# Kernel tuning notes

Measured on AMD Instinct MI355X. Metric: run time of the kernel, lower is better.

## Reference

```python
import jax, jax.numpy as jnp
import numpy as np

STRIDE = 16
SIZES = np.array([128.0, 256.0, 512.0], np.float32)
RATIOS = np.array([0.5, 1.0, 2.0], np.float32)
N_POS, N_NEG = 32, 32          # n_sample=64, pos_ratio=0.5
POS_THR, NEG_THR = 0.7, 0.2
W_CONF, W_REG = 1.0, 5.0


def _conv(x, w, b, stride, pad):
    y = jax.lax.conv_general_dilated(x, w, (stride, stride), [(pad, pad), (pad, pad)],
                                     dimension_numbers=('NCHW', 'OIHW', 'NCHW'))
    return y + b[None, :, None, None]


def _anchors(fw, fh, stride):
    # 9 anchors per center: 3 sizes x 3 aspect ratios
    ws = (SIZES[:, None] * np.sqrt(RATIOS)[None, :]).reshape(-1)
    hs = (SIZES[:, None] / np.sqrt(RATIOS)[None, :]).reshape(-1)
    wh = jnp.asarray(np.stack([ws, hs], -1))                      # (9,2)
    cx = (jnp.arange(fw, dtype=jnp.float32) + 0.5) * stride
    cy = (jnp.arange(fh, dtype=jnp.float32) + 0.5) * stride
    gx, gy = jnp.meshgrid(cx, cy, indexing='ij')                  # x-major, like the torch list comp
    ctr = jnp.stack([gx, gy], -1)[:, :, None, :]                  # (fw,fh,1,2)
    tl = ctr - wh / 2.0
    xywh = jnp.concatenate([tl, jnp.broadcast_to(wh, tl.shape)], -1)  # (fw,fh,9,4)
    return xywh.reshape(-1, 4)


def _xywh_to_xyxy(b):
    return jnp.concatenate([b[:, :2], b[:, :2] + b[:, 2:]], -1)


def _iou(a, b):  # a [N,4], b [M,4], xyxy
    lt = jnp.maximum(a[:, None, :2], b[None, :, :2])
    rb = jnp.minimum(a[:, None, 2:], b[None, :, 2:])
    inter = jnp.clip(rb - lt, 0.0).prod(-1)
    aa = (a[:, 2] - a[:, 0]) * (a[:, 3] - a[:, 1])
    ab = (b[:, 2] - b[:, 0]) * (b[:, 3] - b[:, 1])
    return inter / (aa[:, None] + ab[None, :] - inter)


def _head_flat(y, per):  # [1, 9*per, H, W] -> [W*H*9, per], matching anchor flatten order
    _, _, H, W = y.shape
    return y[0].reshape(9, per, H, W).transpose(3, 2, 0, 1).reshape(-1, per)


def _apply_offsets(boxes, off):  # decode proposals from xyxy boxes + (dx,dy,dw,dh)
    w = boxes[:, 2] - boxes[:, 0]; h = boxes[:, 3] - boxes[:, 1]
    cx = boxes[:, 0] + 0.5 * w;    cy = boxes[:, 1] + 0.5 * h
    ncx = cx + off[:, 0] * w;      ncy = cy + off[:, 1] * h
    nw = w * jnp.exp(off[:, 2]);   nh = h * jnp.exp(off[:, 3])
    return jnp.stack([ncx - nw / 2, ncy - nh / 2, ncx + nw / 2, ncy + nh / 2], -1)


def _box_offset(anc, gt):
    aw = anc[:, 2] - anc[:, 0]; ah = anc[:, 3] - anc[:, 1]
    acx = anc[:, 0] + 0.5 * aw; acy = anc[:, 1] + 0.5 * ah
    gw = gt[:, 2] - gt[:, 0];   gh = gt[:, 3] - gt[:, 1]
    gcx = gt[:, 0] + 0.5 * gw;  gcy = gt[:, 1] + 0.5 * gh
    return jnp.stack([(gcx - acx) / aw, (gcy - acy) / ah,
                      jnp.log(gw / aw), jnp.log(gh / ah)], -1)


def setup_inputs():
    key = jax.random.key(0)
    ks = jax.random.split(key, 12)
    img_data = jax.random.normal(ks[0], (1, 3, 1600, 1600), jnp.float32)
    x1 = jax.random.uniform(ks[1], (64,), minval=0.0, maxval=1400.0)
    y1 = jax.random.uniform(ks[2], (64,), minval=0.0, maxval=1400.0)
    bw = jax.random.uniform(ks[3], (64,), minval=32.0, maxval=200.0)
    bh = jax.random.uniform(ks[4], (64,), minval=32.0, maxval=200.0)
    gt_boxes = jnp.stack([x1, y1, x1 + bw, y1 + bh], -1)[None]   # [1,64,4], all valid (no -1 pad)
    gt_classes = jax.random.randint(ks[5], (1, 64), 1, 21, jnp.int32)
    def w(k, shape, fan):
        return jax.random.normal(k, shape, jnp.float32) * np.float32(np.sqrt(2.0 / fan))
    return dict(
        img_data=img_data, gt_boxes=gt_boxes, gt_classes=gt_classes,
        w1=w(ks[6], (64, 3, 7, 7), 3 * 49),      b1=jnp.zeros(64, jnp.float32),
        w2=w(ks[7], (256, 64, 3, 3), 64 * 9),    b2=jnp.zeros(256, jnp.float32),
        w_rpn=w(ks[8], (256, 256, 3, 3), 256 * 9), b_rpn=jnp.zeros(256, jnp.float32),
        w_cls=w(ks[9], (18, 256, 1, 1), 256),    b_cls=jnp.zeros(18, jnp.float32),
        w_reg=w(ks[10], (36, 256, 1, 1), 256),   b_reg=jnp.zeros(36, jnp.float32),
    )


def reference(img_data, gt_boxes, gt_classes, w1, b1, w2, b2, w_rpn, b_rpn, w_cls, b_cls, w_reg, b_reg):
    # --- feature extractor (total stride 16) ---
    fm = jax.nn.relu(_conv(img_data, w1, b1, 4, 3))
    fm = jax.nn.relu(_conv(fm, w2, b2, 4, 1))            # [1,256,100,100]
    H, W = fm.shape[2], fm.shape[3]
    # --- anchors + IoU matching ---
    anchors_xywh = _anchors(W, H, STRIDE)                # [N,4] xywh
    anchors_xyxy = _xywh_to_xyxy(anchors_xywh)
    gt = gt_boxes[0]                                     # [M,4], all valid
    ious = _iou(anchors_xyxy, gt)                        # [N,M]
    N = ious.shape[0]
    gt_max = ious.max(0)                                 # best iou per gt
    is_gt_best = (ious == gt_max[None, :]).any(1)        # torch: where(iou == gt_max)[0]
    anc_argmax = ious.argmax(1)
    anc_max = ious.max(1)
    labels = jnp.full((N,), -1.0, jnp.float32)
    labels = jnp.where(anc_max < NEG_THR, 0.0, labels)
    labels = jnp.where(is_gt_best, 1.0, labels)
    labels = jnp.where(anc_max > POS_THR, 1.0, labels)
    # --- deterministic pos/neg sampling (fixed sizes; replaces randperm subsampling) ---
    idx = jnp.arange(N, dtype=jnp.float32)
    _, pos_index = jax.lax.top_k(jnp.where(labels == 1.0, anc_max, -1.0), N_POS)
    _, neg_index = jax.lax.top_k(jnp.where(labels == 0.0, 1e6 - idx, -1e9), N_NEG)
    bboxes_pos = anchors_xyxy[pos_index]                 # box_convert(xywh->xyxy) of pos anchors
    # --- proposal module (RPN head) ---
    h = jax.nn.relu(_conv(fm, w_rpn, b_rpn, 1, 1))
    cls = _head_flat(_conv(h, w_cls, b_cls, 1, 0), 2)    # [N,2]
    reg = _head_flat(_conv(h, w_reg, b_reg, 1, 0), 4)    # [N,4]
    pos_score = cls[pos_index]
    neg_score = cls[neg_index]
    offset_pos = reg[pos_index]
    proposals = _apply_offsets(bboxes_pos, offset_pos)
    # --- losses ---
    gt_offset = _box_offset(bboxes_pos, gt[anc_argmax[pos_index]])
    logits = jnp.concatenate([pos_score, neg_score], 0)  # [64,2]
    tgt = jnp.concatenate([jnp.ones(N_POS, jnp.int32), jnp.zeros(N_NEG, jnp.int32)])
    logp = jax.nn.log_softmax(logits, -1)
    cls_loss = -logp[jnp.arange(N_POS + N_NEG), tgt].mean()
    d = gt_offset - offset_pos
    ad = jnp.abs(d)
    reg_loss = jnp.where(ad < 1.0, 0.5 * d * d, ad - 0.5).mean()
    total_rpn_loss = W_CONF * cls_loss + W_REG * reg_loss
    gt_cls_pos = gt_classes[0][anc_argmax[pos_index]]
    return (total_rpn_loss, fm, proposals, pos_index, gt_cls_pos)
```

## Files before the change

kernel.cpp:

```cpp
#include <hip/hip_runtime.h>
#include <math.h>


#define CAP 4096

typedef __attribute__((ext_vector_type(8))) short bf16x8;
typedef __attribute__((ext_vector_type(4))) float f32x4;

__device__ __forceinline__ void dma16(const void* g, void* l) {
    __builtin_amdgcn_global_load_lds((const __attribute__((address_space(1))) void*)g,
                                     (__attribute__((address_space(3))) void*)l, 16, 0, 0);
}

#define OFF_F1T     0
#define OFF_FMT     5171328
#define OFF_CPART   6503040
#define OFF_RPART   7223040
#define OFF_WA1     8663040
#define OFF_W9_2    8672448
#define OFF_W9_3    8746176
#define OFF_WTC     9041088
#define OFF_WTG     9045696
#define OFF_AARG    9054912
#define OFF_NEGM    9144912
#define OFF_POSM    9147728
#define OFF_GTMAX   9150544
#define OFF_CANDS   9150688
#define OFF_CANDI   9154784
#define OFF_IMGB    9158880

__device__ __forceinline__ unsigned short f2bf(float f) {
    unsigned int u = __float_as_uint(f);
    u += 0x7fffu + ((u >> 16) & 1u);
    return (unsigned short)(u >> 16);
}

__device__ __forceinline__ void anchor_box(int i, float& x0, float& y0,
                                           float& x1, float& y1, float& area) {
#pragma clang fp contract(off)
    const float sizes[3]  = {128.f, 256.f, 512.f};
    const float ratios[3] = {0.5f, 1.f, 2.f};
    int a = i % 9;
    int q = i / 9;
    int iy = q % 100;
    int ix = q / 100;
    int s = a / 3, r = a % 3;
    float sq = sqrtf(ratios[r]);
    float w = sizes[s] * sq;
    float h = sizes[s] / sq;
    float cx = ((float)ix + 0.5f) * 16.0f;
    float cy = ((float)iy + 0.5f) * 16.0f;
    x0 = cx - w * 0.5f;
    y0 = cy - h * 0.5f;
    x1 = x0 + w;
    y1 = y0 + h;
    area = (x1 - x0) * (y1 - y0);
}

__device__ __forceinline__ float iou_one(float ax0, float ay0, float ax1, float ay1, float aa,
                                         float bx0, float by0, float bx1, float by1, float ab) {
#pragma clang fp contract(off)
    float ltx = fmaxf(ax0, bx0), lty = fmaxf(ay0, by0);
    float rbx = fminf(ax1, bx1), rby = fminf(ay1, by1);
    float iw = fmaxf(rbx - ltx, 0.0f);
    float ih = fmaxf(rby - lty, 0.0f);
    float inter = iw * ih;
    return inter / ((aa + ab) - inter);
}

__global__ __launch_bounds__(256) void setup_kernel(const float* __restrict__ wc, float* __restrict__ wtc,
                                                    const float* __restrict__ wg, float* __restrict__ wtg,
                                                    const float* __restrict__ w1, unsigned short* __restrict__ wa1,
                                                    const float* __restrict__ w2, unsigned short* __restrict__ w9_2,
                                                    const float* __restrict__ wr, unsigned short* __restrict__ w9_3,
                                                    unsigned int* __restrict__ f1t_u, unsigned int* __restrict__ fmt_u,
                                                    unsigned int* __restrict__ gtmax,
                                                    const float* __restrict__ img, unsigned short* __restrict__ imgb) {
    int i = blockIdx.x * 256 + threadIdx.x;
    if (i < 65) { gtmax[i] = 0u; return; }
    i -= 65;
    if (i < 103040) {
        if (i < 51328) {
            int p = i >> 5, part = i & 31;
            int x, y;
            if (p < 804) { y = (p < 402) ? 0 : 401; x = p % 402; }
            else { int j = p - 804; x = (j < 400) ? 0 : 401; y = 1 + (j % 400); }
            f1t_u[(y * 402 + x) * 32 + part] = 0u;
        } else {
            int i2 = i - 51328;
            int p = i2 >> 7, part = i2 & 127;
            int x, y;
            if (p < 204) { y = (p < 102) ? 0 : 101; x = p % 102; }
            else { int j = p - 204; x = (j < 100) ? 0 : 101; y = 1 + (j % 100); }
            fmt_u[(y * 102 + x) * 128 + part] = 0u;
        }
        return;
    }
    i -= 103040;
    if (i < 4608) { int c = i / 256, k = i - c * 256; wtc[k * 18 + c] = wc[i]; return; }
    i -= 4608;
    if (i < 9216) { int c = i / 256, k = i - c * 256; wtg[k * 36 + c] = wg[i]; return; }
    i -= 9216;
    if (i < 12288) {
        int oc = i / 192, k = i - oc * 192;
        int q = k >> 3, kx = k & 7;
        int ky = q / 3, ic = q - (q / 3) * 3;
        wa1[i] = (q < 21 && kx < 7) ? f2bf(w1[oc * 147 + ic * 49 + ky * 7 + kx])
                                    : (unsigned short)0;
        return;
    }
    i -= 12288;
    if (i < 147456) {
        int unit = i >> 13;
        int rem = i & 8191;
        int ocT = rem >> 9;
        int rem2 = rem & 511;
        int lane = rem2 >> 3;
        int e = rem2 & 7;
        int cc = unit >> 1, kcl = unit & 1;
        int oc = ocT * 16 + (lane & 15);
        int ic = kcl * 32 + (lane >> 4) * 8 + e;
        w9_2[i] = f2bf(w2[(oc * 64 + ic) * 9 + cc]);
        return;
    }
    i -= 147456;
    if (i < 589824) {
        int unit = i >> 13;
        int rem = i & 8191;
        int ocT = rem >> 9;
        int rem2 = rem & 511;
        int lane = rem2 >> 3;
        int e = rem2 & 7;
        int cc = unit >> 1, kcl = unit & 1;
        int kk = cc >> 2, chv = cc & 3;
        int oc = ocT * 16 + (lane & 15);
        int icl = kcl * 32 + (lane >> 4) * 8 + e;
        w9_3[i] = f2bf(wr[(oc * 256 + chv * 64 + icl) * 9 + kk]);
        return;
    }
    i -= 589824;
    if (i < 974448) {
        int ic = i / 324816;
        int rem = i - ic * 324816;
        int row = rem / 202;
        int k = rem - row * 202;
        int y = row - 3;
        bool yok = (y >= 0) && (y < 1600);
        int yc = min(max(y, 0), 1599);
        const float* srow = img + ((size_t)(ic * 1600 + yc)) * 1600;
        unsigned int d[4];
#pragma unroll
        for (int e2 = 0; e2 < 4; e2++) {
            int x0 = k * 8 + 2 * e2 - 11;
            int x1 = x0 + 1;
            bool ok0 = yok && (x0 >= 0) && (x0 < 1600);
            bool ok1 = yok && (x1 >= 0) && (x1 < 1600);
            float f0 = srow[min(max(x0, 0), 1599)];
            float f1 = srow[min(max(x1, 0), 1599)];
            unsigned int lo = ok0 ? (unsigned int)f2bf(f0) : 0u;
            unsigned int hi = ok1 ? (unsigned int)f2bf(f1) : 0u;
            d[e2] = lo | (hi << 16);
        }
        *(uint4*)(imgb + ((size_t)(ic * 1608 + row)) * 1616 + k * 8) =
            make_uint4(d[0], d[1], d[2], d[3]);
    }
}

__device__ __forceinline__ void iou1_body(int bid, int t, const float* __restrict__ gt,
                                          int* __restrict__ aarg, unsigned int* __restrict__ gtmax) {
    __shared__ float sg1[64][4];
    __shared__ float sarea1[64];
    __shared__ unsigned int smax1[64];
    if (t < 64) {
#pragma clang fp contract(off)
        float b0 = gt[t * 4 + 0], b1 = gt[t * 4 + 1];
        float b2 = gt[t * 4 + 2], b3 = gt[t * 4 + 3];
        sg1[t][0] = b0; sg1[t][1] = b1; sg1[t][2] = b2; sg1[t][3] = b3;
        sarea1[t] = (b2 - b0) * (b3 - b1);
        smax1[t] = 0u;
    }
    __syncthreads();
    int i = bid * 256 + t;
    int iq = min(i, 89999);
    float x0, y0, x1, y1, aa;
    anchor_box(iq, x0, y0, x1, y1, aa);
    float best = -1.f;
    int bestj = 0;
    for (int j = 0; j < 64; j++) {
        float v = iou_one(x0, y0, x1, y1, aa, sg1[j][0], sg1[j][1], sg1[j][2], sg1[j][3], sarea1[j]);
        if (v > best) { best = v; bestj = j; }
        if (v > __uint_as_float(smax1[j])) atomicMax(&smax1[j], __float_as_uint(v));
    }
    if (i < 90000) aarg[i] = bestj;
    __syncthreads();
    if (t < 64) atomicMax(&gtmax[t], smax1[t]);
}

__device__ __forceinline__ void iou2_body(int bid, int t, const float* __restrict__ gt,
                                          const unsigned int* __restrict__ gtmax,
                                          unsigned long long* __restrict__ negmask,
                                          unsigned long long* __restrict__ posmask,
                                          float* __restrict__ cand_s, int* __restrict__ cand_i,
                                          unsigned int* __restrict__ cnt) {
    __shared__ float sg2[64][4];
    __shared__ float sarea2[64];
    __shared__ float sgm2[64];
    if (t < 64) {
#pragma clang fp contract(off)
        float b0 = gt[t * 4 + 0], b1 = gt[t * 4 + 1];
        float b2 = gt[t * 4 + 2], b3 = gt[t * 4 + 3];
        sg2[t][0] = b0; sg2[t][1] = b1; sg2[t][2] = b2; sg2[t][3] = b3;
        sarea2[t] = (b2 - b0) * (b3 - b1);
        sgm2[t] = __uint_as_float(gtmax[t]);
    }
    __syncthreads();
    int i = bid * 512 + t;
    if (i >= 90000) return;
    float x0, y0, x1, y1, aa;
    anchor_box(i, x0, y0, x1, y1, aa);
    float best = -1.f;
    bool isbest = false;
    for (int j = 0; j < 64; j++) {
        float v = iou_one(x0, y0, x1, y1, aa, sg2[j][0], sg2[j][1], sg2[j][2], sg2[j][3], sarea2[j]);
        if (v > best) best = v;
        if (v == sgm2[j]) isbest = true;
    }
    float label = -1.f;
    if (best < 0.2f) label = 0.f;
    if (isbest) label = 1.f;
    if (best > 0.7f) label = 1.f;
    unsigned long long negb = __ballot(label == 0.f);
    unsigned long long posb = __ballot(label == 1.f);
    if ((t & 63) == 0) { negmask[i >> 6] = negb; posmask[i >> 6] = posb; }
    if (label == 1.f) {
        unsigned int p = atomicAdd(cnt, 1u);
        if (p < CAP) { cand_s[p] = best; cand_i[p] = i; }
    }
}

__device__ __forceinline__ void conv1_body(int bx, int oy, int t,
                                           const unsigned short* __restrict__ imgb,
                                           const unsigned short* __restrict__ wA,
                                           const float* __restrict__ bias,
                                           unsigned short* __restrict__ f1t) {
    __shared__ __align__(16) unsigned char smem[13312];
    unsigned short* win = (unsigned short*)smem;
    unsigned short* tileT = (unsigned short*)smem;
    int wave = t >> 6, lane = t & 63;
    int quad = lane >> 4, l16 = lane & 15;
    int ox0 = bx * 64;
    int col0 = ox0 * 4 + 8;
    int gy0 = 4 * oy - 3;

    for (int o = wave; o < 13; o += 4) {
        int q = o * 64 + lane;
        int r = q / 33;
        int c = q - r * 33;
        int rc = min(r, 20);
        int ky = rc / 3, ic = rc - (rc / 3) * 3;
        int yp = gy0 + ky + 3;
        size_t offm = ((size_t)(ic * 1608 + yp)) * 1616 + col0 + c * 8;
        size_t offz = (size_t)(q - 693) * 8;
        dma16(imgb + ((r < 21) ? offm : offz), (char*)smem + o * 1024);
    }
    bf16x8 afr[6];
    {
        const bf16x8* ap = (const bf16x8*)(wA + (wave * 16 + l16) * 192 + quad * 8);
#pragma unroll
        for (int c = 0; c < 6; c++) afr[c] = ap[c * 4];
    }
    __syncthreads();

    f32x4 acc[4];
#pragma unroll
    for (int j = 0; j < 4; j++) acc[j] = (f32x4){0.f, 0.f, 0.f, 0.f};
#pragma unroll
    for (int ch = 0; ch < 6; ch++) {
        const unsigned short* wrow = win + (ch * 4 + quad) * 264;
#pragma unroll
        for (int j = 0; j < 4; j++) {
            int px = j * 16 + l16;
            const unsigned long long* bp = (const unsigned long long*)(wrow + 4 * px);
            union { unsigned long long u[2]; bf16x8 v; } uu;
            uu.u[0] = bp[0];
            uu.u[1] = bp[1];
            acc[j] = __builtin_amdgcn_mfma_f32_16x16x32_bf16(afr[ch], uu.v, acc[j], 0, 0, 0);
        }
    }
    __syncthreads();
#pragma unroll
    for (int reg = 0; reg < 4; reg++) {
        int oc = wave * 16 + quad * 4 + reg;
        float bv = bias[oc];
#pragma unroll
        for (int j = 0; j < 4; j++) {
            int px = j * 16 + l16;
            tileT[px * 72 + oc] = f2bf(fmaxf(acc[j][reg] + bv, 0.f));
        }
    }
    __syncthreads();
    int px = t >> 2, part = t & 3;
    int ox = ox0 + px;
    if (ox < 400) {
        int row = (oy + 1) * 402 + ox + 1;
        uint4 v0 = *(const uint4*)(tileT + px * 72 + part * 16);
        uint4 v1 = *(const uint4*)(tileT + px * 72 + part * 16 + 8);
        *(uint4*)(f1t + row * 64 + part * 16) = v0;
        *(uint4*)(f1t + row * 64 + part * 16 + 8) = v1;
    }
}

__global__ __launch_bounds__(256, 4) void conv1_iou1(const unsigned short* __restrict__ imgb,
                                                     const unsigned short* __restrict__ wA,
                                                     const float* __restrict__ bias,
                                                     unsigned short* __restrict__ f1t,
                                                     const float* __restrict__ gt,
                                                     int* __restrict__ aarg,
                                                     unsigned int* __restrict__ gtmax) {
    int t = threadIdx.x;
    if (blockIdx.x < 7) {
        conv1_body(blockIdx.x, blockIdx.y, t, imgb, wA, bias, f1t);
    } else {
        int bid = blockIdx.y;
        if (bid < 352) iou1_body(bid, t, gt, aarg, gtmax);
    }
}

template<int ICC, int RS, int S, bool WRT, bool HEAD>
__device__ __forceinline__ void conv_body(int xs, int y, int t,
                                          const unsigned short* __restrict__ Bt,
                                          const unsigned short* __restrict__ A9,
                                          const float* __restrict__ bias,
                                          float* __restrict__ outF,
                                          unsigned short* __restrict__ outT,
                                          const float* __restrict__ wtc,
                                          const float* __restrict__ wtg,
                                          float* __restrict__ cpart,
                                          float* __restrict__ rpart) {
    constexpr int NC = ICC / 64;
    constexpr int HC = S * 24 + 3;
    constexpr int CHW = ICC / 8;
    constexpr int TOT = 3 * HC * CHW;
    constexpr int BOPS = (TOT + 63) / 64;
    constexpr int BB = BOPS * 1024;
    constexpr int NS = (NC == 1) ? 18 : 72;
    __shared__ __align__(16) unsigned char smem[BB + 49152];
    unsigned short* blds = (unsigned short*)smem;
    float* hlds = (float*)(smem + BB);

    int wave = t >> 6, lane = t & 63;
    int ow = wave & 3, ph = wave >> 2;
    int quad = lane >> 4, l16 = lane & 15;
    int oc0 = ow * 64;
    int pl = ph * 16 + l16;
    int pxe = min(pl, 24);
    int swp = pxe & 7;

    for (int o = wave; o < BOPS; o += 8) {
        int q = min(o * 64 + lane, TOT - 1);
        int row = q / CHW;
        int e = q - row * CHW;
        int ky = row / HC;
        int c = row - ky * HC;
        int sz = (S == 4) ? (e ^ ((c >> 2) & 7)) : (e ^ (row & 7));
        dma16(Bt + ((size_t)(S * y + ky) * RS + S * xs * 25 + c) * ICC + sz * 8,
              (char*)smem + o * 1024);
    }
    {
        char* s0 = (char*)smem + BB;
        dma16(A9 + (size_t)(wave * 64 + lane) * 8, s0 + wave * 1024);
        dma16(A9 + (size_t)((wave + 8) * 64 + lane) * 8, s0 + (wave + 8) * 1024);
        if (NS > 1) {
            char* s1 = (char*)smem + BB + 16384;
            const unsigned short* a1 = A9 + 8192;
            dma16(a1 + (size_t)(wave * 64 + lane) * 8, s1 + wave * 1024);
            dma16(a1 + (size_t)((wave + 8) * 64 + lane) * 8, s1 + (wave + 8) * 1024);
        }
    }

    f32x4 acc[4];
#pragma unroll
    for (int mt = 0; mt < 4; mt++) acc[mt] = (f32x4){0.f, 0.f, 0.f, 0.f};
    __syncthreads();

    for (int u = 0; u < NS; u++) {
        const unsigned short* ab = (const unsigned short*)(smem + BB + (u % 3) * 16384);
        int cc = u >> 1, kcl = u & 1;
        int pass = cc / NC, ch = cc - pass * NC;
        int ky = pass / 3, kx = pass - (pass / 3) * 3;
        int row = ky * HC + S * pxe + kx;
        int ck = kcl * 4 + quad;
        int chunk = (S == 4) ? (ck ^ swp) : ((ch * 8 + ck) ^ (row & 7));
        bf16x8 bf = *(const bf16x8*)(blds + row * ICC + chunk * 8);
#pragma unroll
        for (int mt = 0; mt < 4; mt++) {
            bf16x8 af = *(const bf16x8*)(ab + ((ow * 4 + mt) * 64 + lane) * 8);
            acc[mt] = __builtin_amdgcn_mfma_f32_16x16x32_bf16(af, bf, acc[mt], 0, 0, 0);
        }
        if (u + 2 < NS) {
            char* dst = (char*)smem + BB + ((u + 2) % 3) * 16384;
            const unsigned short* src = A9 + (size_t)(u + 2) * 8192;
            dma16(src + (size_t)(wave * 64 + lane) * 8, dst + wave * 1024);
            dma16(src + (size_t)((wave + 8) * 64 + lane) * 8, dst + (wave + 8) * 1024);
        }
        if (u + 1 < NS) {
            if (u + 2 < NS) asm volatile("s_waitcnt vmcnt(2)" ::: "memory");
            else            asm volatile("s_waitcnt vmcnt(0)" ::: "memory");
            __builtin_amdgcn_s_barrier();
            __builtin_amdgcn_sched_barrier(0);
        }
    }

    if (HEAD) __syncthreads();

#pragma unroll
    for (int mt = 0; mt < 4; mt++) {
#pragma unroll
        for (int reg = 0; reg < 4; reg++) {
            int oc = oc0 + mt * 16 + quad * 4 + reg;
            float bv = bias[oc];
            if (pl < 25) {
                float v = fmaxf(acc[mt][reg] + bv, 0.f);
                if (HEAD) {
                    hlds[oc * 26 + pl] = v;
                } else {
                    int p = y * 100 + xs * 25 + pl;
                    outF[oc * 10000 + p] = v;
                    if (WRT) {
                        int r = (y + 1) * 102 + xs * 25 + pl + 1;
                        outT[r * 256 + oc] = f2bf(v);
                    }
                }
            }
        }
    }
    if (HEAD) {
        __syncthreads();
        int base = y * 100 + xs * 25;
        for (int it = t; it < 5400; it += 512) {
            int ch = it / 1350;
            int r = it - ch * 1350;
            int j = r / 25;
            int p = r - j * 25;
            int jc = (j < 18) ? j : (j - 18);
            const float* wt = (j < 18) ? (wtc + jc) : (wtg + jc);
            int stride = (j < 18) ? 18 : 36;
            int ic0 = ch * 64;
            float acc2 = 0.f;
#pragma unroll 8
            for (int ic = 0; ic < 64; ic++)
                acc2 += hlds[(ic0 + ic) * 26 + p] * wt[(ic0 + ic) * stride];
            float* dst = (j < 18) ? (cpart + (ch * 18 + jc) * 10000)
                                  : (rpart + (ch * 36 + jc) * 10000);
            dst[base + p] = acc2;
        }
    }
}

__global__ __launch_bounds__(512) void conv2_iou2(const unsigned short* __restrict__ Bt,
                                                  const unsigned short* __restrict__ A9,
                                                  const float* __restrict__ bias,
                                                  float* __restrict__ outF,
                                                  unsigned short* __restrict__ outT,
                                                  const float* __restrict__ gt,
                                                  const unsigned int* __restrict__ gtmax,
                                                  unsigned long long* __restrict__ negmask,
                                                  unsigned long long* __restrict__ posmask,
                                                  float* __restrict__ cand_s,
                                                  int* __restrict__ cand_i,
                                                  unsigned int* __restrict__ cnt) {
    int t = threadIdx.x;
    if (blockIdx.x < 4) {
        conv_body<64, 402, 4, true, false>(blockIdx.x, blockIdx.y, t, Bt, A9, bias,
                                           outF, outT, nullptr, nullptr, nullptr, nullptr);
    } else {
        int bid = (blockIdx.x - 4) * 100 + blockIdx.y;
        if (bid < 176) iou2_body(bid, t, gt, gtmax, negmask, posmask, cand_s, cand_i, cnt);
    }
}

__global__ __launch_bounds__(512) void conv3_head(const unsigned short* __restrict__ Bt,
                                                  const unsigned short* __restrict__ A9,
                                                  const float* __restrict__ bias,
                                                  const float* __restrict__ wtc,
                                                  const float* __restrict__ wtg,
                                                  float* __restrict__ cpart,
                                                  float* __restrict__ rpart) {
    conv_body<256, 102, 1, false, true>(blockIdx.x, blockIdx.y, threadIdx.x, Bt, A9, bias,
                                        nullptr, nullptr, wtc, wtg, cpart, rpart);
}

__device__ __forceinline__ unsigned long long shflx64(unsigned long long v, int m) {
    int lo = __shfl_xor((int)(unsigned)(v & 0xFFFFFFFFull), m);
    int hi = __shfl_xor((int)(unsigned)(v >> 32), m);
    return ((unsigned long long)(unsigned)hi << 32) | (unsigned)lo;
}

__device__ int wave_first32(const unsigned long long* __restrict__ mask,
                            bool invert, int* __restrict__ outIdx, int lane) {
    const int NW = 1407;
    const int WPT = 22;
    unsigned long long mw[WPT];
    int cnt = 0;
#pragma unroll
    for (int u = 0; u < WPT; u++) {
        int w = lane * WPT + u;
        unsigned long long m = 0ull;
        if (w < NW) {
            m = mask[w];
            if (invert) m = ~m;
            if (w == NW - 1) m &= 0xFFFFull;
        }
        mw[u] = m;
        cnt += __builtin_popcountll(m);
    }
    int inc = cnt;
#pragma unroll
    for (int off = 1; off < 64; off <<= 1) {
        int v = __shfl_up(inc, off);
        if (lane >= off) inc += v;
    }
    int total = __shfl(inc, 63);
    int pref = inc - cnt;
    if (pref < 32) {
#pragma unroll
        for (int u = 0; u < WPT; u++) {
            unsigned long long m = mw[u];
            int wbase = (lane * WPT + u) * 64;
            while (m && pref < 32) {
                int b = __builtin_ctzll(m);
                outIdx[pref++] = wbase + b;
                m &= m - 1;
            }
        }
    }
    return total;
}

__global__ __launch_bounds__(64) void tail_kernel(const unsigned long long* __restrict__ negmask,
                                                  const unsigned long long* __restrict__ posmask,
                                                  const float* __restrict__ cand_s,
                                                  const int* __restrict__ cand_i,
                                                  const unsigned int* __restrict__ cnt,
                                                  const float* __restrict__ cpart,
                                                  const float* __restrict__ rpart,
                                                  const float* __restrict__ bcls,
                                                  const float* __restrict__ breg,
                                                  const int* __restrict__ aarg,
                                                  const float* __restrict__ gt,
                                                  const int* __restrict__ gtc,
                                                  float* __restrict__ out) {
    __shared__ unsigned long long keys[CAP + 32];
    __shared__ int sfill[32];
    __shared__ int spidx[32];
    __shared__ int snidx[32];
    int lane = threadIdx.x;

    int ncand = min((int)*cnt, CAP);
    for (int c = lane; c < ncand; c += 64) {
        unsigned u = __float_as_uint(cand_s[c]);
        u ^= (u & 0x80000000u) ? 0xFFFFFFFFu : 0x80000000u;
        keys[c] = ((unsigned long long)u << 32) | (0xFFFFFFFFu - (unsigned)cand_i[c]);
    }
    int ntot = ncand;
    if (ncand < 32) {
        int tot = wave_first32(posmask, true, sfill, lane);
        int nfill = min(tot, 32);
        unsigned um1 = __float_as_uint(-1.0f) ^ 0xFFFFFFFFu;
        for (int k2 = lane; k2 < nfill; k2 += 64)
            keys[ncand + k2] = ((unsigned long long)um1 << 32) | (0xFFFFFFFFu - (unsigned)sfill[k2]);
        ntot += nfill;
    }

    unsigned long long lk = 0ull; int ls = -1;
    for (int c = lane; c < ntot; c += 64) {
        unsigned long long k = keys[c];
        if (k > lk) { lk = k; ls = c; }
    }
    for (int s = 0; s < 32; s++) {
        unsigned long long mk = lk;
#pragma unroll
        for (int off = 1; off < 64; off <<= 1) {
            unsigned long long o = shflx64(mk, off);
            if (o > mk) mk = o;
        }
        if (lk == mk && mk != 0ull) {
            spidx[s] = (int)(0xFFFFFFFFu - (unsigned)(mk & 0xFFFFFFFFull));
            keys[ls] = 0ull;
            lk = 0ull; ls = -1;
            for (int c = lane; c < ntot; c += 64) {
                unsigned long long k = keys[c];
                if (k > lk) { lk = k; ls = c; }
            }
        }
    }

    int totn = wave_first32(negmask, false, snidx, lane);
    if (lane == 0) {
        int nf = min(totn, 32);
        for (int s = nf; s < 32; s++) snidx[s] = s;
    }

    {
#pragma clang fp contract(off)
        const int PROP_OFF = 1 + 2560000;
        int t = lane;
        int n = (t < 32) ? spidx[t] : snidx[t - 32];
        int a = n % 9;
        int q = n / 9;
        int iy = q % 100;
        int ix = q / 100;
        int p = iy * 100 + ix;

        float l0 = bcls[a * 2 + 0], l1 = bcls[a * 2 + 1];
        for (int c = 0; c < 4; c++) {
            l0 += cpart[(c * 18 + a * 2 + 0) * 10000 + p];
            l1 += cpart[(c * 18 + a * 2 + 1) * 10000 + p];
        }
        float m = fmaxf(l0, l1);
        float lse = m + logf(expf(l0 - m) + expf(l1 - m));
        float logp = ((t < 32) ? l1 : l0) - lse;
        float cls_sum = logp;
#pragma unroll
        for (int off = 32; off > 0; off >>= 1) cls_sum += __shfl_down(cls_sum, off);

        float reg_sum = 0.f;
        if (t < 32) {
            float offv[4];
#pragma unroll
            for (int k = 0; k < 4; k++) {
                float v = breg[a * 4 + k];
                for (int c = 0; c < 4; c++) v += rpart[(c * 36 + a * 4 + k) * 10000 + p];
                offv[k] = v;
            }
            float x0, y0, x1, y1, aa;
            anchor_box(n, x0, y0, x1, y1, aa);
            float w = x1 - x0, h = y1 - y0;
            float cx = x0 + 0.5f * w, cy = y0 + 0.5f * h;
            float ncx = cx + offv[0] * w, ncy = cy + offv[1] * h;
            float nw = w * expf(offv[2]), nh = h * expf(offv[3]);
            out[PROP_OFF + t * 4 + 0] = ncx - nw * 0.5f;
            out[PROP_OFF + t * 4 + 1] = ncy - nh * 0.5f;
            out[PROP_OFF + t * 4 + 2] = ncx + nw * 0.5f;
            out[PROP_OFF + t * 4 + 3] = ncy + nh * 0.5f;

            int j = aarg[n];
            float g0 = gt[j * 4 + 0], g1 = gt[j * 4 + 1];
            float g2 = gt[j * 4 + 2], g3 = gt[j * 4 + 3];
            float gw = g2 - g0, gh = g3 - g1;
            float gcx = g0 + 0.5f * gw, gcy = g1 + 0.5f * gh;
            float tg[4];
            tg[0] = (gcx - cx) / w;
            tg[1] = (gcy - cy) / h;
            tg[2] = logf(gw / w);
            tg[3] = logf(gh / h);
#pragma unroll
            for (int k = 0; k < 4; k++) {
                float d = tg[k] - offv[k];
                float ad = fabsf(d);
                reg_sum += (ad < 1.f) ? 0.5f * d * d : ad - 0.5f;
            }
            out[PROP_OFF + 128 + t] = (float)n;
            out[PROP_OFF + 160 + t] = (float)gtc[j];
        }
#pragma unroll
        for (int off = 32; off > 0; off >>= 1) reg_sum += __shfl_down(reg_sum, off);
        if (t == 0) {
            float cls_loss = -(cls_sum / 64.f);
            float reg_loss = reg_sum / 128.f;
            out[0] = cls_loss + 5.f * reg_loss;
        }
    }
}

extern "C" void kernel_launch(void* const* d_in, const int* in_sizes, int n_in,
                              void* d_out, int out_size, void* d_ws, size_t ws_size,
                              hipStream_t stream) {
    const float* img = (const float*)d_in[0];
    const float* gt  = (const float*)d_in[1];
    const int*   gtc = (const int*)d_in[2];
    const float* w1  = (const float*)d_in[3];
    const float* b1  = (const float*)d_in[4];
    const float* w2  = (const float*)d_in[5];
    const float* b2  = (const float*)d_in[6];
    const float* wr  = (const float*)d_in[7];
    const float* br  = (const float*)d_in[8];
    const float* wc  = (const float*)d_in[9];
    const float* bc  = (const float*)d_in[10];
    const float* wg  = (const float*)d_in[11];
    const float* bg  = (const float*)d_in[12];
    float* out = (float*)d_out;
    float* ws = (float*)d_ws;

    unsigned short* f1t  = (unsigned short*)(ws + OFF_F1T);
    unsigned short* fmt  = (unsigned short*)(ws + OFF_FMT);
    unsigned short* wa1  = (unsigned short*)(ws + OFF_WA1);
    unsigned short* w9_2 = (unsigned short*)(ws + OFF_W9_2);
    unsigned short* w9_3 = (unsigned short*)(ws + OFF_W9_3);
    unsigned short* imgb = (unsigned short*)(ws + OFF_IMGB);
    float* cpart = ws + OFF_CPART;
    float* rpart = ws + OFF_RPART;
    float* wtc   = ws + OFF_WTC;
    float* wtg   = ws + OFF_WTG;
    int*   aarg  = (int*)(ws + OFF_AARG);
    unsigned long long* negm = (unsigned long long*)(ws + OFF_NEGM);
    unsigned long long* posm = (unsigned long long*)(ws + OFF_POSM);
    unsigned int* gtmax = (unsigned int*)(ws + OFF_GTMAX);
    unsigned int* cnt   = gtmax + 64;
    float* cands = ws + OFF_CANDS;
    int*   candi = (int*)(ws + OFF_CANDI);
    float* fm    = out + 1;

    setup_kernel<<<dim3(7192), dim3(256), 0, stream>>>(wc, wtc, wg, wtg, w1, wa1,
                                                       w2, w9_2, wr, w9_3,
                                                       (unsigned int*)f1t, (unsigned int*)fmt, gtmax,
                                                       img, imgb);

    conv1_iou1<<<dim3(8, 400), dim3(256), 0, stream>>>(imgb, wa1, b1, f1t, gt, aarg, gtmax);
    conv2_iou2<<<dim3(6, 100), dim3(512), 0, stream>>>(f1t, w9_2, b2, fm, fmt,
                                                       gt, gtmax, negm, posm, cands, candi, cnt);
    conv3_head<<<dim3(4, 100), dim3(512), 0, stream>>>(fmt, w9_3, br, wtc, wtg, cpart, rpart);
    tail_kernel<<<dim3(1), dim3(64), 0, stream>>>(negm, posm, cands, candi, cnt,
                                                  cpart, rpart, bc, bg, aarg, gt, gtc, out);
}
```

Baseline: 306.1 us.

## Split conv K across wave groups, load weights from global into registers

Changes the conv work split so that the two wave groups split the reduction dimension instead of the pixel rows. Each wave now computes two 16-pixel tiles per weight fragment, reusing the A fragment across both. Weight fragments are read directly from global memory into double-buffered registers instead of being staged through a triple-buffered LDS ring with per-step barriers. Partial sums are combined through shared memory at the end. The weight prepack layout and launch bounds are adjusted to match. This cuts LDS footprint and per-step barriers but adds a cross-wave reduction and relies on global and cache latency for the weight loads.

```diff
diff --git a/kernel.cpp b/kernel.cpp
--- a/kernel.cpp
+++ b/kernel.cpp
@@ -111,13 +111,13 @@
     }
     i -= 12288;
     if (i < 147456) {
-        int unit = i >> 13;
-        int rem = i & 8191;
-        int ocT = rem >> 9;
-        int rem2 = rem & 511;
-        int lane = rem2 >> 3;
+        int cc = i >> 14;
+        int rem = i & 16383;
+        int ocT = rem >> 10;
+        int rem2 = rem & 1023;
+        int kcl = rem2 >> 9;
+        int lane = (rem2 & 511) >> 3;
         int e = rem2 & 7;
-        int cc = unit >> 1, kcl = unit & 1;
         int oc = ocT * 16 + (lane & 15);
         int ic = kcl * 32 + (lane >> 4) * 8 + e;
         w9_2[i] = f2bf(w2[(oc * 64 + ic) * 9 + cc]);
@@ -125,13 +125,13 @@
     }
     i -= 147456;
     if (i < 589824) {
-        int unit = i >> 13;
-        int rem = i & 8191;
-        int ocT = rem >> 9;
-        int rem2 = rem & 511;
-        int lane = rem2 >> 3;
+        int cc = i >> 14;
+        int rem = i & 16383;
+        int ocT = rem >> 10;
+        int rem2 = rem & 1023;
+        int kcl = rem2 >> 9;
+        int lane = (rem2 & 511) >> 3;
         int e = rem2 & 7;
-        int cc = unit >> 1, kcl = unit & 1;
         int kk = cc >> 2, chv = cc & 3;
         int oc = ocT * 16 + (lane & 15);
         int icl = kcl * 32 + (lane >> 4) * 8 + e;
@@ -343,18 +343,20 @@
     constexpr int TOT = 3 * HC * CHW;
     constexpr int BOPS = (TOT + 63) / 64;
     constexpr int BB = BOPS * 1024;
-    constexpr int NS = (NC == 1) ? 18 : 72;
-    __shared__ __align__(16) unsigned char smem[BB + 49152];
+    constexpr int SMB0 = HEAD ? (32768 + 256 * 26 * 4) : BB;
+    constexpr int SMB = (SMB0 < BB) ? BB : SMB0;
+    __shared__ __align__(16) unsigned char smem[SMB];
     unsigned short* blds = (unsigned short*)smem;
-    float* hlds = (float*)(smem + BB);
+    float* sred = (float*)smem;
+    float* hlds = (float*)(smem + 32768);
 
     int wave = t >> 6, lane = t & 63;
-    int ow = wave & 3, ph = wave >> 2;
+    int ow = wave & 3, kg = wave >> 2;
     int quad = lane >> 4, l16 = lane & 15;
     int oc0 = ow * 64;
-    int pl = ph * 16 + l16;
-    int pxe = min(pl, 24);
-    int swp = pxe & 7;
+    int pxe0 = min(l16, 24);
+    int pxe1 = min(16 + l16, 24);
+    int sw0 = pxe0 & 7, sw1 = pxe1 & 7;
 
     for (int o = wave; o < BOPS; o += 8) {
         int q = min(o * 64 + lane, TOT - 1);
@@ -366,69 +368,94 @@
         dma16(Bt + ((size_t)(S * y + ky) * RS + S * xs * 25 + c) * ICC + sz * 8,
               (char*)smem + o * 1024);
     }
+
+    f32x4 acc[4][2];
+#pragma unroll
+    for (int mt = 0; mt < 4; mt++)
+#pragma unroll
+        for (int j = 0; j < 2; j++) acc[mt][j] = (f32x4){0.f, 0.f, 0.f, 0.f};
+
+    const bf16x8* Av = (const bf16x8*)A9;
+    __syncthreads();
+
+    constexpr int NS = (NC == 1) ? 9 : 36;
+    bf16x8 afA[4], afB[4];
     {
-        char* s0 = (char*)smem + BB;
-        dma16(A9 + (size_t)(wave * 64 + lane) * 8, s0 + wave * 1024);
-        dma16(A9 + (size_t)((wave + 8) * 64 + lane) * 8, s0 + (wave + 8) * 1024);
-        if (NS > 1) {
-            char* s1 = (char*)smem + BB + 16384;
-            const unsigned short* a1 = A9 + 8192;
-            dma16(a1 + (size_t)(wave * 64 + lane) * 8, s1 + wave * 1024);
-            dma16(a1 + (size_t)((wave + 8) * 64 + lane) * 8, s1 + (wave + 8) * 1024);
-        }
-    }
-
-    f32x4 acc[4];
-#pragma unroll
-    for (int mt = 0; mt < 4; mt++) acc[mt] = (f32x4){0.f, 0.f, 0.f, 0.f};
-    __syncthreads();
-
-    for (int u = 0; u < NS; u++) {
-        const unsigned short* ab = (const unsigned short*)(smem + BB + (u % 3) * 16384);
-        int cc = u >> 1, kcl = u & 1;
+        int cc0 = (NC == 1) ? 0 : kg * 18;
+        int kl0 = (NC == 1) ? kg : 0;
+#pragma unroll
+        for (int mt = 0; mt < 4; mt++)
+            afA[mt] = Av[(size_t)cc0 * 2048 + (ow * 4 + mt) * 128 + kl0 * 64 + lane];
+    }
+    auto kstep = [&](int s, bf16x8 (&cur)[4], bf16x8 (&nxt)[4]) {
+        int cc  = (NC == 1) ? s : kg * 18 + (s >> 1);
+        int kcl = (NC == 1) ? kg : (s & 1);
         int pass = cc / NC, ch = cc - pass * NC;
         int ky = pass / 3, kx = pass - (pass / 3) * 3;
-        int row = ky * HC + S * pxe + kx;
+        int row0 = ky * HC + S * pxe0 + kx;
+        int row1 = ky * HC + S * pxe1 + kx;
         int ck = kcl * 4 + quad;
-        int chunk = (S == 4) ? (ck ^ swp) : ((ch * 8 + ck) ^ (row & 7));
-        bf16x8 bf = *(const bf16x8*)(blds + row * ICC + chunk * 8);
+        int chunk0 = (S == 4) ? (ck ^ sw0) : ((ch * 8 + ck) ^ (row0 & 7));
+        int chunk1 = (S == 4) ? (ck ^ sw1) : ((ch * 8 + ck) ^ (row1 & 7));
+        bf16x8 bf0 = *(const bf16x8*)(blds + row0 * ICC + chunk0 * 8);
+        bf16x8 bf1 = *(const bf16x8*)(blds + row1 * ICC + chunk1 * 8);
+        if (s + 1 < NS) {
+            int cn = (NC == 1) ? (s + 1) : kg * 18 + ((s + 1) >> 1);
+            int kn = (NC == 1) ? kg : ((s + 1) & 1);
+#pragma unroll
+            for (int mt = 0; mt < 4; mt++)
+                nxt[mt] = Av[(size_t)cn * 2048 + (ow * 4 + mt) * 128 + kn * 64 + lane];
+        }
 #pragma unroll
         for (int mt = 0; mt < 4; mt++) {
-            bf16x8 af = *(const bf16x8*)(ab + ((ow * 4 + mt) * 64 + lane) * 8);
-            acc[mt] = __builtin_amdgcn_mfma_f32_16x16x32_bf16(af, bf, acc[mt], 0, 0, 0);
-        }
-        if (u + 2 < NS) {
-            char* dst = (char*)smem + BB + ((u + 2) % 3) * 16384;
-            const unsigned short* src = A9 + (size_t)(u + 2) * 8192;
-            dma16(src + (size_t)(wave * 64 + lane) * 8, dst + wave * 1024);
-            dma16(src + (size_t)((wave + 8) * 64 + lane) * 8, dst + (wave + 8) * 1024);
-        }
-        if (u + 1 < NS) {
-            if (u + 2 < NS) asm volatile("s_waitcnt vmcnt(2)" ::: "memory");
-            else            asm volatile("s_waitcnt vmcnt(0)" ::: "memory");
-            __builtin_amdgcn_s_barrier();
-            __builtin_amdgcn_sched_barrier(0);
-        }
-    }
-
-    if (HEAD) __syncthreads();
-
-#pragma unroll
-    for (int mt = 0; mt < 4; mt++) {
-#pragma unroll
-        for (int reg = 0; reg < 4; reg++) {
-            int oc = oc0 + mt * 16 + quad * 4 + reg;
-            float bv = bias[oc];
-            if (pl < 25) {
-                float v = fmaxf(acc[mt][reg] + bv, 0.f);
-                if (HEAD) {
-                    hlds[oc * 26 + pl] = v;
-                } else {
-                    int p = y * 100 + xs * 25 + pl;
-                    outF[oc * 10000 + p] = v;
-                    if (WRT) {
-                        int r = (y + 1) * 102 + xs * 25 + pl + 1;
-                        outT[r * 256 + oc] = f2bf(v);
+            acc[mt][0] = __builtin_amdgcn_mfma_f32_16x16x32_bf16(cur[mt], bf0, acc[mt][0], 0, 0, 0);
+            acc[mt][1] = __builtin_amdgcn_mfma_f32_16x16x32_bf16(cur[mt], bf1, acc[mt][1], 0, 0, 0);
+        }
+    };
+#pragma unroll
+    for (int s2 = 0; s2 < NS; s2 += 2) {
+        kstep(s2, afA, afB);
+        if (s2 + 1 < NS) kstep(s2 + 1, afB, afA);
+    }
+
+    __syncthreads();
+    if (kg == 1) {
+#pragma unroll
+        for (int mt = 0; mt < 4; mt++)
+#pragma unroll
+            for (int j = 0; j < 2; j++)
+                *(f32x4*)(sred + ((((ow * 4 + mt) * 2 + j) * 64 + lane) * 4)) = acc[mt][j];
+    }
+    __syncthreads();
+    if (kg == 0) {
+#pragma unroll
+        for (int mt = 0; mt < 4; mt++)
+#pragma unroll
+            for (int j = 0; j < 2; j++) {
+                f32x4 o = *(const f32x4*)(sred + ((((ow * 4 + mt) * 2 + j) * 64 + lane) * 4));
+                acc[mt][j] = acc[mt][j] + o;
+            }
+#pragma unroll
+        for (int mt = 0; mt < 4; mt++) {
+#pragma unroll
+            for (int reg = 0; reg < 4; reg++) {
+                int oc = oc0 + mt * 16 + quad * 4 + reg;
+                float bv = bias[oc];
+#pragma unroll
+                for (int j = 0; j < 2; j++) {
+                    int pl = j * 16 + l16;
+                    if (pl < 25) {
+                        float v = fmaxf(acc[mt][j][reg] + bv, 0.f);
+                        if (HEAD) {
+                            hlds[oc * 26 + pl] = v;
+                        } else {
+                            int p = y * 100 + xs * 25 + pl;
+                            outF[oc * 10000 + p] = v;
+                            if (WRT) {
+                                int r = (y + 1) * 102 + xs * 25 + pl + 1;
+                                outT[r * 256 + oc] = f2bf(v);
+                            }
+                        }
                     }
                 }
             }
@@ -457,18 +484,18 @@
     }
 }
 
-__global__ __launch_bounds__(512) void conv2_iou2(const unsigned short* __restrict__ Bt,
-                                                  const unsigned short* __restrict__ A9,
-                                                  const float* __restrict__ bias,
-                                                  float* __restrict__ outF,
-                                                  unsigned short* __restrict__ outT,
-                                                  const float* __restrict__ gt,
-                                                  const unsigned int* __restrict__ gtmax,
-                                                  unsigned long long* __restrict__ negmask,
-                                                  unsigned long long* __restrict__ posmask,
-                                                  float* __restrict__ cand_s,
-                                                  int* __restrict__ cand_i,
-                                                  unsigned int* __restrict__ cnt) {
+__global__ __launch_bounds__(512, 4) void conv2_iou2(const unsigned short* __restrict__ Bt,
+                                                     const unsigned short* __restrict__ A9,
+                                                     const float* __restrict__ bias,
+                                                     float* __restrict__ outF,
+                                                     unsigned short* __restrict__ outT,
+                                                     const float* __restrict__ gt,
+                                                     const unsigned int* __restrict__ gtmax,
+                                                     unsigned long long* __restrict__ negmask,
+                                                     unsigned long long* __restrict__ posmask,
+                                                     float* __restrict__ cand_s,
+                                                     int* __restrict__ cand_i,
+                                                     unsigned int* __restrict__ cnt) {
     int t = threadIdx.x;
     if (blockIdx.x < 4) {
         conv_body<64, 402, 4, true, false>(blockIdx.x, blockIdx.y, t, Bt, A9, bias,
@@ -479,13 +506,13 @@
     }
 }
 
-__global__ __launch_bounds__(512) void conv3_head(const unsigned short* __restrict__ Bt,
-                                                  const unsigned short* __restrict__ A9,
-                                                  const float* __restrict__ bias,
-                                                  const float* __restrict__ wtc,
-                                                  const float* __restrict__ wtg,
-                                                  float* __restrict__ cpart,
-                                                  float* __restrict__ rpart) {
+__global__ __launch_bounds__(512, 4) void conv3_head(const unsigned short* __restrict__ Bt,
+                                                     const unsigned short* __restrict__ A9,
+                                                     const float* __restrict__ bias,
+                                                     const float* __restrict__ wtc,
+                                                     const float* __restrict__ wtg,
+                                                     float* __restrict__ cpart,
+                                                     float* __restrict__ rpart) {
     conv_body<256, 102, 1, false, true>(blockIdx.x, blockIdx.y, threadIdx.x, Bt, A9, bias,
                                         nullptr, nullptr, wtc, wtg, cpart, rpart);
 }
```

New measurement: 270.5 us. 1.13x faster.
